# Kernel tuning notes

Measured on AMD Instinct MI355X. Metric: run time of the kernel, lower is better.

Reference implementation:

```python
import jax, jax.numpy as jnp
import numpy as np

N, D, H, L = 100000, 128, 4, 2
C = D // H  # per-head channels
E = 1600000
NEG_SLOPE = 0.2
LN_EPS = 1e-5


def setup_inputs() -> dict:
    key = jax.random.key(0)
    ks = jax.random.split(key, 8)
    x = jax.random.normal(ks[0], (N, D), dtype=jnp.float32)
    edge_index = jax.random.randint(ks[1], (2, E), 0, N, dtype=jnp.int64)
    s = 1.0 / np.sqrt(D)
    Wl = jax.random.normal(ks[2], (L, D, D), dtype=jnp.float32) * s
    Wr = jax.random.normal(ks[3], (L, D, D), dtype=jnp.float32) * s
    att = jax.random.normal(ks[4], (L, H, C), dtype=jnp.float32) * (1.0 / np.sqrt(C))
    bias = jnp.zeros((L, D), dtype=jnp.float32)
    gamma = jnp.ones((L, D), dtype=jnp.float32)
    beta = jnp.zeros((L, D), dtype=jnp.float32)
    return {"x": x, "edge_index": edge_index, "Wl": Wl, "Wr": Wr,
            "att": att, "bias": bias, "gamma": gamma, "beta": beta}


def _gatv2_layer(h, src, dst, Wl, Wr, att, bias):
    # h: (N, D); src/dst: (E2,) with self-loops already appended
    xl = (h @ Wl).reshape(N, H, C)  # source-side transform
    xr = (h @ Wr).reshape(N, H, C)  # target-side transform
    e = jax.nn.leaky_relu(xl[src] + xr[dst], NEG_SLOPE)      # (E2, H, C)
    alpha = jnp.einsum('ehc,hc->eh', e, att)                 # (E2, H)
    # segment softmax over incoming edges of each destination node
    m = jax.ops.segment_max(alpha, dst, num_segments=N)      # (N, H)
    ea = jnp.exp(alpha - m[dst])
    s = jax.ops.segment_sum(ea, dst, num_segments=N)         # (N, H)
    a = ea / s[dst]                                          # (E2, H)
    out = jax.ops.segment_sum(a[:, :, None] * xl[src], dst, num_segments=N)
    return out.reshape(N, D) + bias


def _layer_norm(y, gamma, beta):
    mu = jnp.mean(y, axis=-1, keepdims=True)
    var = jnp.var(y, axis=-1, keepdims=True)
    return (y - mu) * jax.lax.rsqrt(var + LN_EPS) * gamma + beta


def reference(x, edge_index, Wl, Wr, att, bias, gamma, beta):
    # PyG GATv2Conv defaults: add_self_loops=True (eval mode: dropouts identity)
    loops = jnp.arange(N, dtype=edge_index.dtype)
    src = jnp.concatenate([edge_index[0], loops])
    dst = jnp.concatenate([edge_index[1], loops])
    h = x
    for l in range(L):
        g = _gatv2_layer(h, src, dst, Wl[l], Wr[l], att[l], bias[l])
        h = h + jax.nn.elu(_layer_norm(g, gamma[l], beta[l]))
    return h
```

## Files before the change

### kernel.cpp

```cpp
#include <hip/hip_runtime.h>
#include <hip/hip_fp16.h>
#include <math.h>

#define N_NODES 100000
#define D_FEAT  128
#define E_EDGES 1600000
#define E2      (E_EDGES + N_NODES)
#define NEG_SLOPE 0.2f
#define LN_EPS    1e-5f

#define NB   391
#define TS   8192
#define NTIL ((E2 + TS - 1) / TS)

typedef __attribute__((ext_vector_type(4))) float floatx4;
typedef _Float16 h2 __attribute__((ext_vector_type(2)));
typedef _Float16 h8 __attribute__((ext_vector_type(8)));

static __device__ __forceinline__ float fdot2f(h2 a, h2 b, float c) {
#if __has_builtin(__builtin_amdgcn_fdot2)
    return __builtin_amdgcn_fdot2(a, b, c, false);
#else
    return (float)a[0] * (float)b[0] + (float)a[1] * (float)b[1] + c;
#endif
}

static __device__ __forceinline__ h2 shfl_xor_h2(h2 v, int off) {
    int i = __builtin_bit_cast(int, v);
    i = __shfl_xor(i, off);
    return __builtin_bit_cast(h2, i);
}

__global__ __launch_bounds__(1024) void tile_count(const int* __restrict__ edge_dst,
                                                   int* __restrict__ tcnt,
                                                   unsigned short* __restrict__ rankbuf) {
    __shared__ int h[NB];
    const int t = threadIdx.x;
    if (t < NB) h[t] = 0;
    __syncthreads();
    const int base = blockIdx.x * TS;
#pragma unroll
    for (int j = 0; j < TS / 1024; ++j) {
        int i = base + j * 1024 + t;
        if (i < E2) {
            int d = (i < E_EDGES) ? edge_dst[i] : (i - E_EDGES);
            int rk = atomicAdd(&h[d >> 8], 1);
            rankbuf[i] = (unsigned short)rk;
        }
    }
    __syncthreads();
    if (t < NB) tcnt[blockIdx.x * NB + t] = h[t];
}

__global__ __launch_bounds__(256) void col_scan(const int* __restrict__ tcnt,
                                                int* __restrict__ toff,
                                                int* __restrict__ bcnt) {
    __shared__ int s[256];
    const int b = blockIdx.x;
    const int t = threadIdx.x;
    int v = (t < NTIL) ? tcnt[t * NB + b] : 0;
    s[t] = v;
    __syncthreads();
    for (int off = 1; off < 256; off <<= 1) {
        int x = (t >= off) ? s[t - off] : 0;
        __syncthreads();
        s[t] += x;
        __syncthreads();
    }
    if (t < NTIL) toff[t * NB + b] = s[t] - v;
    if (t == 255) bcnt[b] = s[255];
}

__global__ __launch_bounds__(512) void bucket_scan(const int* __restrict__ bcnt,
                                                   int* __restrict__ bstart,
                                                   int* __restrict__ rowstart) {
    __shared__ int s[512];
    const int t = threadIdx.x;
    int v = (t < NB) ? bcnt[t] : 0;
    s[t] = v;
    __syncthreads();
    for (int off = 1; off < 512; off <<= 1) {
        int x = (t >= off) ? s[t - off] : 0;
        __syncthreads();
        s[t] += x;
        __syncthreads();
    }
    if (t <= NB) bstart[t] = s[t] - v;
    if (t == 0) rowstart[N_NODES] = E2;
}

__global__ __launch_bounds__(1024) void tile_scatter(const int* __restrict__ edge_src,
                                                     const int* __restrict__ edge_dst,
                                                     const int* __restrict__ bstart,
                                                     const int* __restrict__ toff,
                                                     const unsigned short* __restrict__ rankbuf,
                                                     unsigned* __restrict__ pairbuf) {
    __shared__ int base[NB];
    const int t = threadIdx.x;
    if (t < NB) base[t] = bstart[t] + toff[blockIdx.x * NB + t];
    __syncthreads();
    const int tb = blockIdx.x * TS;
#pragma unroll
    for (int j = 0; j < TS / 1024; ++j) {
        int i = tb + j * 1024 + t;
        if (i < E2) {
            int d, sr;
            if (i < E_EDGES) { d = edge_dst[i]; sr = edge_src[i]; }
            else             { d = i - E_EDGES; sr = d; }
            int b = d >> 8;
            int pos = base[b] + (int)rankbuf[i];
            pairbuf[pos] = (unsigned)sr | ((unsigned)(d & 255) << 17);
        }
    }
}

__global__ __launch_bounds__(1024) void bucketize(const unsigned* __restrict__ pairbuf,
                                                  const int* __restrict__ bstart,
                                                  int* __restrict__ rowstart,
                                                  int* __restrict__ csr_src) {
    __shared__ int cnt[256], off[256];
    const int blk = blockIdx.x;
    const int t = threadIdx.x;
    const int nbase = blk << 8;
    if (t < 256) cnt[t] = 0;
    __syncthreads();
    const int e0 = bstart[blk], e1 = bstart[blk + 1];

    unsigned pr0, pr1, pr2, pr3, pr4, pr5, pr6, pr7;
    int rk0, rk1, rk2, rk3, rk4, rk5, rk6, rk7;
#define LOADP(K, PR)  { int p = e0 + t + (K) * 1024; PR = (p < e1) ? pairbuf[p] : 0u; }
    LOADP(0, pr0) LOADP(1, pr1) LOADP(2, pr2) LOADP(3, pr3)
    LOADP(4, pr4) LOADP(5, pr5) LOADP(6, pr6) LOADP(7, pr7)
#undef LOADP
#define HIST(K, PR, RK) { int p = e0 + t + (K) * 1024; \
        RK = (p < e1) ? atomicAdd(&cnt[PR >> 17], 1) : 0; }
    HIST(0, pr0, rk0) HIST(1, pr1, rk1) HIST(2, pr2, rk2) HIST(3, pr3, rk3)
    HIST(4, pr4, rk4) HIST(5, pr5, rk5) HIST(6, pr6, rk6) HIST(7, pr7, rk7)
#undef HIST
    __syncthreads();

    int v = (t < 256) ? cnt[t] : 0;
    __shared__ int sc[256];
    if (t < 256) sc[t] = v;
    __syncthreads();
    for (int o = 1; o < 256; o <<= 1) {
        int x = (t < 256 && t >= o) ? sc[t - o] : 0;
        __syncthreads();
        if (t < 256) sc[t] += x;
        __syncthreads();
    }
    if (t < 256) {
        int excl = sc[t] - v;
        int node = nbase + t;
        if (node < N_NODES) rowstart[node] = e0 + excl;
        off[t] = e0 + excl;
    }
    __syncthreads();

#define SCAT(K, PR, RK) { int p = e0 + t + (K) * 1024; \
        if (p < e1) csr_src[off[PR >> 17] + RK] = (int)(PR & 0x1FFFF); }
    SCAT(0, pr0, rk0) SCAT(1, pr1, rk1) SCAT(2, pr2, rk2) SCAT(3, pr3, rk3)
    SCAT(4, pr4, rk4) SCAT(5, pr5, rk5) SCAT(6, pr6, rk6) SCAT(7, pr7, rk7)
#undef SCAT
}

__global__ void prep_wt(const float* __restrict__ Wl, const float* __restrict__ Wr,
                        const float* __restrict__ att,
                        _Float16* __restrict__ Wt, _Float16* __restrict__ atth) {
    int idx = blockIdx.x * 256 + threadIdx.x;
    if (idx < 65536) {
        int l    = idx >> 15;
        int rem  = idx & 32767;
        int side = rem >> 14;
        int cw   = rem & 16383;
        int col  = cw >> 7, k = cw & 127;
        const float* W = side ? Wr : Wl;
        Wt[idx] = (_Float16)W[l * 16384 + k * 128 + col];
    } else if (idx < 65536 + 256) {
        int j = idx - 65536;
        atth[j] = (_Float16)att[j];
    }
}

__global__ __launch_bounds__(256) void gemm_mfma5(
        const _Float16* __restrict__ hA,
        const float* __restrict__ Afp,
        const _Float16* __restrict__ Wt,
        _Float16* __restrict__ xl, _Float16* __restrict__ xr, int n_rows) {
    __shared__ char bsm[65536];
    const int tid  = threadIdx.x;
    const int wave = tid >> 6;
    const int lane = tid & 63;
    const int m = lane & 15;
    const int q = lane >> 4;
    const int r0 = (blockIdx.x * 4 + wave) * 32;

#pragma unroll
    for (int k = 0; k < 16; ++k) {
        int ci  = tid + k * 256;
        int row = ci >> 4;
        int off = (ci & 15) << 4;
        uint4 v = *(const uint4*)((const char*)Wt + row * 256 + off);
        *(uint4*)(bsm + row * 256 + (off ^ ((row & 7) << 4))) = v;
    }
    __syncthreads();

    int arow0 = r0 + m;        if (arow0 >= n_rows) arow0 = n_rows - 1;
    int arow1 = r0 + 16 + m;   if (arow1 >= n_rows) arow1 = n_rows - 1;

    floatx4 acc[2][2][8];
#pragma unroll
    for (int s = 0; s < 2; ++s)
#pragma unroll
        for (int rt = 0; rt < 2; ++rt)
#pragma unroll
            for (int ct = 0; ct < 8; ++ct) acc[s][rt][ct] = (floatx4){0.f,0.f,0.f,0.f};

    const int swz = (m & 7) << 4;
#pragma unroll
    for (int ks = 0; ks < 4; ++ks) {
        const int k0 = ks * 32 + q * 8;
        const int cb = k0 * 2;
        h8 a0, a1;
        if (Afp) {
            float4 f0 = *(const float4*)(Afp + (size_t)arow0 * 128 + k0);
            float4 f1 = *(const float4*)(Afp + (size_t)arow0 * 128 + k0 + 4);
            float4 g0 = *(const float4*)(Afp + (size_t)arow1 * 128 + k0);
            float4 g1 = *(const float4*)(Afp + (size_t)arow1 * 128 + k0 + 4);
            a0 = (h8){(_Float16)f0.x, (_Float16)f0.y, (_Float16)f0.z, (_Float16)f0.w,
                      (_Float16)f1.x, (_Float16)f1.y, (_Float16)f1.z, (_Float16)f1.w};
            a1 = (h8){(_Float16)g0.x, (_Float16)g0.y, (_Float16)g0.z, (_Float16)g0.w,
                      (_Float16)g1.x, (_Float16)g1.y, (_Float16)g1.z, (_Float16)g1.w};
        } else {
            a0 = *(const h8*)(hA + (size_t)arow0 * 128 + k0);
            a1 = *(const h8*)(hA + (size_t)arow1 * 128 + k0);
        }
#pragma unroll
        for (int s = 0; s < 2; ++s) {
#pragma unroll
            for (int ct = 0; ct < 8; ++ct) {
                int row = s * 128 + ct * 16 + m;
                h8 b = *(const h8*)(bsm + row * 256 + (cb ^ swz));
                acc[s][0][ct] = __builtin_amdgcn_mfma_f32_16x16x32_f16(a0, b, acc[s][0][ct], 0, 0, 0);
                acc[s][1][ct] = __builtin_amdgcn_mfma_f32_16x16x32_f16(a1, b, acc[s][1][ct], 0, 0, 0);
            }
        }
    }

#pragma unroll
    for (int s = 0; s < 2; ++s) {
        _Float16* out = s ? xr : xl;
#pragma unroll
        for (int rt = 0; rt < 2; ++rt)
#pragma unroll
            for (int ct = 0; ct < 8; ++ct)
#pragma unroll
                for (int i = 0; i < 4; ++i) {
                    int row = r0 + rt * 16 + q * 4 + i;
                    if (row < n_rows)
                        out[(size_t)row * 128 + ct * 16 + m] = (_Float16)acc[s][rt][ct][i];
                }
    }
}

union U16 { uint4 u; h2 h[4]; };

__global__ __launch_bounds__(256) void gat_node10(
        const _Float16* __restrict__ xl,
        const _Float16* __restrict__ xr,
        const float* __restrict__ h_in_f32,
        const _Float16* __restrict__ h_in_f16,
        const int* __restrict__ rowstart, const int* __restrict__ csr_src,
        const _Float16* __restrict__ atth, const float* __restrict__ bias,
        const float* __restrict__ gamma, const float* __restrict__ beta,
        float* __restrict__ out_f32,
        _Float16* __restrict__ out_f16) {
    const int wave = threadIdx.x >> 6;
    const int lane = threadIdx.x & 63;
    const int node = blockIdx.x * 4 + wave;
    const int esub = lane >> 3;
    const int r    = lane & 7;
    const int c0   = r * 16;
    const int c    = c0 + 2 * esub;

    const int p0 = rowstart[node], p1 = rowstart[node + 1];
    const int pe = p1 - 1;

    U16 xra, xrb, ata, atb;
    {
        const uint4* xp = (const uint4*)(xr + (size_t)node * 128 + c0);
        xra.u = xp[0]; xrb.u = xp[1];
        const uint4* ap = (const uint4*)(atth + c0);
        ata.u = ap[0]; atb.u = ap[1];
    }
    const float2 bi = *(const float2*)(bias + c);
    const h2 ns2 = {(_Float16)NEG_SLOPE, (_Float16)NEG_SLOPE};

    const unsigned short* xls = (const unsigned short*)xl;

    float s = 0.f;
    h2 acc2[8];
#pragma unroll
    for (int j = 0; j < 8; ++j) acc2[j] = (h2){(_Float16)0.f, (_Float16)0.f};

    auto consume = [&](const U16& u0, const U16& u1, bool v) {
        float da = 0.f, db = 0.f;
#pragma unroll
        for (int qq = 0; qq < 4; ++qq) {
            h2 z  = u0.h[qq] + xra.h[qq];
            h2 lk = __builtin_elementwise_max(z, z * ns2);
            da = fdot2f(lk, ata.h[qq], da);
        }
#pragma unroll
        for (int qq = 0; qq < 4; ++qq) {
            h2 z  = u1.h[qq] + xrb.h[qq];
            h2 lk = __builtin_elementwise_max(z, z * ns2);
            db = fdot2f(lk, atb.h[qq], db);
        }
        float d = da + db;
        float alpha = d + __shfl_xor(d, 1);
        float w = v ? __expf(alpha) : 0.f;
        s += w;
        h2 w2 = {(_Float16)w, (_Float16)w};
#pragma unroll
        for (int qq = 0; qq < 4; ++qq)
            acc2[qq] = w2 * u0.h[qq] + acc2[qq];
#pragma unroll
        for (int qq = 0; qq < 4; ++qq)
            acc2[qq + 4] = w2 * u1.h[qq] + acc2[qq + 4];
    };

    int pA = p0 + esub;        if (pA > pe) pA = pe;
    int pB = p0 + 8 + esub;    if (pB > pe) pB = pe;
    int pC = p0 + 16 + esub;   if (pC > pe) pC = pe;
    int i0 = csr_src[pA];
    int i1 = csr_src[pB];
    int i2 = csr_src[pC];

    U16 s0a, s0b, s1a, s1b, s2a, s2b;
    { const uint4* rp = (const uint4*)(xls + (size_t)i0 * 128 + c0); s0a.u = rp[0]; s0b.u = rp[1]; }
    { const uint4* rp = (const uint4*)(xls + (size_t)i1 * 128 + c0); s1a.u = rp[0]; s1b.u = rp[1]; }

    int pb = p0;
    for (;;) {
        {
            int pn = pb + 24 + esub; if (pn > pe) pn = pe;
            int inew = csr_src[pn];
            if (pb + 16 < p1) {
                const uint4* rp = (const uint4*)(xls + (size_t)i2 * 128 + c0);
                s2a.u = rp[0]; s2b.u = rp[1];
            }
            consume(s0a, s0b, (pb + esub) < p1);
            i0 = inew;
            pb += 8; if (pb >= p1) break;
        }
        {
            int pn = pb + 24 + esub; if (pn > pe) pn = pe;
            int inew = csr_src[pn];
            if (pb + 16 < p1) {
                const uint4* rp = (const uint4*)(xls + (size_t)i0 * 128 + c0);
                s0a.u = rp[0]; s0b.u = rp[1];
            }
            consume(s1a, s1b, (pb + esub) < p1);
            i1 = inew;
            pb += 8; if (pb >= p1) break;
        }
        {
            int pn = pb + 24 + esub; if (pn > pe) pn = pe;
            int inew = csr_src[pn];
            if (pb + 16 < p1) {
                const uint4* rp = (const uint4*)(xls + (size_t)i1 * 128 + c0);
                s1a.u = rp[0]; s1b.u = rp[1];
            }
            consume(s2a, s2b, (pb + esub) < p1);
            i2 = inew;
            pb += 8; if (pb >= p1) break;
        }
    }

    float ssum = s;
    ssum += __shfl_xor(ssum, 8);
    ssum += __shfl_xor(ssum, 16);
    ssum += __shfl_xor(ssum, 32);

    const bool sel0 = (esub & 1) != 0;
    const bool sel1 = ((esub >> 1) & 1) != 0;
    const bool sel2 = ((esub >> 2) & 1) != 0;
    h2 b4[4];
#pragma unroll
    for (int k = 0; k < 4; ++k) {
        h2 keep = sel0 ? acc2[2 * k + 1] : acc2[2 * k];
        h2 send = sel0 ? acc2[2 * k]     : acc2[2 * k + 1];
        b4[k] = keep + shfl_xor_h2(send, 8);
    }
    h2 c2[2];
#pragma unroll
    for (int k = 0; k < 2; ++k) {
        h2 keep = sel1 ? b4[2 * k + 1] : b4[2 * k];
        h2 send = sel1 ? b4[2 * k]     : b4[2 * k + 1];
        c2[k] = keep + shfl_xor_h2(send, 16);
    }
    h2 keepf = sel2 ? c2[1] : c2[0];
    h2 sendf = sel2 ? c2[0] : c2[1];
    h2 tot = keepf + shfl_xor_h2(sendf, 32);

    const float invS = 1.f / ssum;
    float g0 = (float)tot[0] * invS + bi.x;
    float g1 = (float)tot[1] * invS + bi.y;

    const float2 ga = *(const float2*)(gamma + c);
    const float2 be = *(const float2*)(beta + c);
    float hx, hy;
    if (h_in_f16) {
        h2 hv = *(const h2*)(h_in_f16 + (size_t)node * 128 + c);
        hx = (float)hv[0]; hy = (float)hv[1];
    } else {
        float2 hv = *(const float2*)(h_in_f32 + (size_t)node * 128 + c);
        hx = hv.x; hy = hv.y;
    }

    float sum = g0 + g1, sq = g0 * g0 + g1 * g1;
#pragma unroll
    for (int off = 1; off < 64; off <<= 1) {
        sum += __shfl_xor(sum, off);
        sq  += __shfl_xor(sq, off);
    }
    float mu   = sum * (1.f / 128.f);
    float var  = sq * (1.f / 128.f) - mu * mu;
    float rstd = rsqrtf(var + LN_EPS);
    float y0 = (g0 - mu) * rstd * ga.x + be.x;
    float y1 = (g1 - mu) * rstd * ga.y + be.y;
    float e0 = (y0 > 0.f) ? y0 : (__expf(y0) - 1.f);
    float e1 = (y1 > 0.f) ? y1 : (__expf(y1) - 1.f);

    float ox = hx + e0;
    float oy = hy + e1;
    if (out_f32) {
        float2 o; o.x = ox; o.y = oy;
        *(float2*)(out_f32 + (size_t)node * 128 + c) = o;
    } else {
        h2 po = {(_Float16)ox, (_Float16)oy};
        *(h2*)(out_f16 + (size_t)node * 128 + c) = po;
    }
}

extern "C" void kernel_launch(void* const* d_in, const int* in_sizes, int n_in,
                              void* d_out, int out_size, void* d_ws, size_t ws_size,
                              hipStream_t stream) {
    const float* x     = (const float*)d_in[0];
    const int*   eidx  = (const int*)d_in[1];
    const float* Wl    = (const float*)d_in[2];
    const float* Wr    = (const float*)d_in[3];
    const float* att   = (const float*)d_in[4];
    const float* bias  = (const float*)d_in[5];
    const float* gamma = (const float*)d_in[6];
    const float* beta  = (const float*)d_in[7];
    float* out = (float*)d_out;

    char* ws = (char*)d_ws;
    _Float16* xl = (_Float16*)ws;              ws += (size_t)N_NODES * 128 * 2;
    _Float16* xr = (_Float16*)ws;              ws += (size_t)N_NODES * 128 * 2;
    _Float16* h16 = (_Float16*)ws;             ws += (size_t)N_NODES * 128 * 2;
    _Float16* Wt  = (_Float16*)ws;             ws += (size_t)65536 * 2;
    _Float16* atth = (_Float16*)ws;            ws += 256 * 2;
    unsigned* pairbuf = (unsigned*)ws;         ws += (size_t)E2 * 4;
    unsigned short* rankbuf = (unsigned short*)ws; ws += (size_t)E2 * 2;
    int* tcnt     = (int*)ws; ws += (size_t)NTIL * NB * 4;
    int* toff     = (int*)ws; ws += (size_t)NTIL * NB * 4;
    int* bcnt     = (int*)ws; ws += (NB + 1) * 4;
    int* bstart   = (int*)ws; ws += (NB + 1) * 4;
    int* rowstart = (int*)ws; ws += (size_t)(N_NODES + 4) * 4;
    int* csr_src  = (int*)ws; ws += (size_t)E2 * 4;

    const int* edge_src = eidx;
    const int* edge_dst = eidx + E_EDGES;

    prep_wt<<<257, 256, 0, stream>>>(Wl, Wr, att, Wt, atth);

    tile_count<<<NTIL, 1024, 0, stream>>>(edge_dst, tcnt, rankbuf);
    col_scan<<<NB, 256, 0, stream>>>(tcnt, toff, bcnt);
    bucket_scan<<<1, 512, 0, stream>>>(bcnt, bstart, rowstart);
    tile_scatter<<<NTIL, 1024, 0, stream>>>(edge_src, edge_dst, bstart, toff,
                                            rankbuf, pairbuf);
    bucketize<<<NB, 1024, 0, stream>>>(pairbuf, bstart, rowstart, csr_src);

    const int gemm_gx = (N_NODES + 127) / 128;
    for (int l = 0; l < 2; ++l) {
        gemm_mfma5<<<gemm_gx, 256, 0, stream>>>(
            (l == 0) ? nullptr : h16, (l == 0) ? x : nullptr,
            Wt + (size_t)l * 32768, xl, xr, N_NODES);
        gat_node10<<<N_NODES / 4, 256, 0, stream>>>(
            xl, xr,
            (l == 0) ? x : nullptr, (l == 0) ? nullptr : h16,
            rowstart, csr_src,
            atth + l * 128, bias + l * 128, gamma + l * 128, beta + l * 128,
            (l == 1) ? out : nullptr, (l == 0) ? h16 : nullptr);
    }
}
```

Measured before the change: 364.7 us.

## Fuse CSR build and weight prep into one cooperative kernel with grid syncs

Replaces six small kernels (weight conversion, tile count, column scan, bucket scan, tile scatter, bucketize) with a single cooperative launch of 256 blocks of 1024 threads that uses grid.sync between phases. This removes five kernel launches and their inter-kernel gaps from the preprocessing stage. In exchange, the bucket loops now run over 256 persistent blocks instead of 391, the column scan uses a 1024-wide scan in place of a 256-wide one, and the kernel depends on all 256 blocks being co-resident.

```diff
diff --git a/kernel.cpp b/kernel.cpp
--- a/kernel.cpp
+++ b/kernel.cpp
@@ -1,6 +1,9 @@
 #include <hip/hip_runtime.h>
 #include <hip/hip_fp16.h>
+#include <hip/hip_cooperative_groups.h>
 #include <math.h>
+
+namespace cg = cooperative_groups;
 
 #define N_NODES 100000
 #define D_FEAT  128
@@ -31,154 +34,142 @@
     return __builtin_bit_cast(h2, i);
 }
 
-__global__ __launch_bounds__(1024) void tile_count(const int* __restrict__ edge_dst,
-                                                   int* __restrict__ tcnt,
-                                                   unsigned short* __restrict__ rankbuf) {
-    __shared__ int h[NB];
+__global__ __launch_bounds__(1024) void csr_fused(
+        const int* __restrict__ edge_src, const int* __restrict__ edge_dst,
+        const float* __restrict__ Wl, const float* __restrict__ Wr,
+        const float* __restrict__ att,
+        _Float16* __restrict__ Wt, _Float16* __restrict__ atth,
+        int* __restrict__ tcnt, int* __restrict__ toff,
+        int* __restrict__ bcnt, int* __restrict__ bstart,
+        unsigned short* __restrict__ rankbuf, unsigned* __restrict__ pairbuf,
+        int* __restrict__ rowstart, int* __restrict__ csr_src) {
+    cg::grid_group grid = cg::this_grid();
+    __shared__ int sh[1024];
+    __shared__ int sh2[256];
     const int t = threadIdx.x;
-    if (t < NB) h[t] = 0;
-    __syncthreads();
-    const int base = blockIdx.x * TS;
-#pragma unroll
-    for (int j = 0; j < TS / 1024; ++j) {
-        int i = base + j * 1024 + t;
-        if (i < E2) {
-            int d = (i < E_EDGES) ? edge_dst[i] : (i - E_EDGES);
-            int rk = atomicAdd(&h[d >> 8], 1);
-            rankbuf[i] = (unsigned short)rk;
-        }
-    }
-    __syncthreads();
-    if (t < NB) tcnt[blockIdx.x * NB + t] = h[t];
-}
-
-__global__ __launch_bounds__(256) void col_scan(const int* __restrict__ tcnt,
-                                                int* __restrict__ toff,
-                                                int* __restrict__ bcnt) {
-    __shared__ int s[256];
     const int b = blockIdx.x;
-    const int t = threadIdx.x;
-    int v = (t < NTIL) ? tcnt[t * NB + b] : 0;
-    s[t] = v;
-    __syncthreads();
-    for (int off = 1; off < 256; off <<= 1) {
-        int x = (t >= off) ? s[t - off] : 0;
-        __syncthreads();
-        s[t] += x;
-        __syncthreads();
-    }
-    if (t < NTIL) toff[t * NB + b] = s[t] - v;
-    if (t == 255) bcnt[b] = s[255];
-}
-
-__global__ __launch_bounds__(512) void bucket_scan(const int* __restrict__ bcnt,
-                                                   int* __restrict__ bstart,
-                                                   int* __restrict__ rowstart) {
-    __shared__ int s[512];
-    const int t = threadIdx.x;
-    int v = (t < NB) ? bcnt[t] : 0;
-    s[t] = v;
-    __syncthreads();
-    for (int off = 1; off < 512; off <<= 1) {
-        int x = (t >= off) ? s[t - off] : 0;
-        __syncthreads();
-        s[t] += x;
-        __syncthreads();
-    }
-    if (t <= NB) bstart[t] = s[t] - v;
-    if (t == 0) rowstart[N_NODES] = E2;
-}
-
-__global__ __launch_bounds__(1024) void tile_scatter(const int* __restrict__ edge_src,
-                                                     const int* __restrict__ edge_dst,
-                                                     const int* __restrict__ bstart,
-                                                     const int* __restrict__ toff,
-                                                     const unsigned short* __restrict__ rankbuf,
-                                                     unsigned* __restrict__ pairbuf) {
-    __shared__ int base[NB];
-    const int t = threadIdx.x;
-    if (t < NB) base[t] = bstart[t] + toff[blockIdx.x * NB + t];
-    __syncthreads();
-    const int tb = blockIdx.x * TS;
-#pragma unroll
-    for (int j = 0; j < TS / 1024; ++j) {
-        int i = tb + j * 1024 + t;
-        if (i < E2) {
-            int d, sr;
-            if (i < E_EDGES) { d = edge_dst[i]; sr = edge_src[i]; }
-            else             { d = i - E_EDGES; sr = d; }
-            int b = d >> 8;
-            int pos = base[b] + (int)rankbuf[i];
-            pairbuf[pos] = (unsigned)sr | ((unsigned)(d & 255) << 17);
-        }
-    }
-}
-
-__global__ __launch_bounds__(1024) void bucketize(const unsigned* __restrict__ pairbuf,
-                                                  const int* __restrict__ bstart,
-                                                  int* __restrict__ rowstart,
-                                                  int* __restrict__ csr_src) {
-    __shared__ int cnt[256], off[256];
-    const int blk = blockIdx.x;
-    const int t = threadIdx.x;
-    const int nbase = blk << 8;
-    if (t < 256) cnt[t] = 0;
-    __syncthreads();
-    const int e0 = bstart[blk], e1 = bstart[blk + 1];
-
-    unsigned pr0, pr1, pr2, pr3, pr4, pr5, pr6, pr7;
-    int rk0, rk1, rk2, rk3, rk4, rk5, rk6, rk7;
+
+    {
+        int gid = b * 1024 + t;
+        if (gid < 65536) {
+            int l = gid >> 15, rem = gid & 32767, side = rem >> 14, cw = rem & 16383;
+            int col = cw >> 7, k = cw & 127;
+            const float* W = side ? Wr : Wl;
+            Wt[gid] = (_Float16)W[l * 16384 + k * 128 + col];
+        } else if (gid < 65536 + 256) {
+            atth[gid - 65536] = (_Float16)att[gid - 65536];
+        }
+    }
+
+    if (b < NTIL) {
+        if (t < NB) sh[t] = 0;
+        __syncthreads();
+        const int base = b * TS;
+#pragma unroll
+        for (int j = 0; j < TS / 1024; ++j) {
+            int i = base + j * 1024 + t;
+            if (i < E2) {
+                int d = (i < E_EDGES) ? edge_dst[i] : (i - E_EDGES);
+                int rk = atomicAdd(&sh[d >> 8], 1);
+                rankbuf[i] = (unsigned short)rk;
+            }
+        }
+        __syncthreads();
+        if (t < NB) tcnt[b * NB + t] = sh[t];
+    }
+    grid.sync();
+
+    for (int bk = b; bk < NB; bk += 256) {
+        int v = (t < NTIL) ? tcnt[t * NB + bk] : 0;
+        sh[t] = v;
+        __syncthreads();
+        for (int off = 1; off < 1024; off <<= 1) {
+            int x = (t >= off) ? sh[t - off] : 0;
+            __syncthreads();
+            sh[t] += x;
+            __syncthreads();
+        }
+        if (t < NTIL) toff[t * NB + bk] = sh[t] - v;
+        if (t == 1023) bcnt[bk] = sh[1023];
+        __syncthreads();
+    }
+    grid.sync();
+
+    if (b == 0) {
+        int v = (t < NB) ? bcnt[t] : 0;
+        sh[t] = v;
+        __syncthreads();
+        for (int off = 1; off < 1024; off <<= 1) {
+            int x = (t >= off) ? sh[t - off] : 0;
+            __syncthreads();
+            sh[t] += x;
+            __syncthreads();
+        }
+        if (t <= NB) bstart[t] = sh[t] - v;
+        if (t == 0) rowstart[N_NODES] = E2;
+    }
+    grid.sync();
+
+    if (b < NTIL) {
+        if (t < NB) sh[t] = bstart[t] + toff[b * NB + t];
+        __syncthreads();
+        const int tb = b * TS;
+#pragma unroll
+        for (int j = 0; j < TS / 1024; ++j) {
+            int i = tb + j * 1024 + t;
+            if (i < E2) {
+                int d, sr;
+                if (i < E_EDGES) { d = edge_dst[i]; sr = edge_src[i]; }
+                else             { d = i - E_EDGES; sr = d; }
+                int bk = d >> 8;
+                pairbuf[sh[bk] + (int)rankbuf[i]] =
+                    (unsigned)sr | ((unsigned)(d & 255) << 17);
+            }
+        }
+    }
+    grid.sync();
+
+    for (int bk = b; bk < NB; bk += 256) {
+        if (t < 256) sh[t] = 0;
+        __syncthreads();
+        const int e0 = bstart[bk], e1 = bstart[bk + 1];
+
+        unsigned pr0, pr1, pr2, pr3, pr4, pr5, pr6, pr7;
+        int rk0, rk1, rk2, rk3, rk4, rk5, rk6, rk7;
 #define LOADP(K, PR)  { int p = e0 + t + (K) * 1024; PR = (p < e1) ? pairbuf[p] : 0u; }
-    LOADP(0, pr0) LOADP(1, pr1) LOADP(2, pr2) LOADP(3, pr3)
-    LOADP(4, pr4) LOADP(5, pr5) LOADP(6, pr6) LOADP(7, pr7)
+        LOADP(0, pr0) LOADP(1, pr1) LOADP(2, pr2) LOADP(3, pr3)
+        LOADP(4, pr4) LOADP(5, pr5) LOADP(6, pr6) LOADP(7, pr7)
 #undef LOADP
 #define HIST(K, PR, RK) { int p = e0 + t + (K) * 1024; \
-        RK = (p < e1) ? atomicAdd(&cnt[PR >> 17], 1) : 0; }
-    HIST(0, pr0, rk0) HIST(1, pr1, rk1) HIST(2, pr2, rk2) HIST(3, pr3, rk3)
-    HIST(4, pr4, rk4) HIST(5, pr5, rk5) HIST(6, pr6, rk6) HIST(7, pr7, rk7)
+        RK = (p < e1) ? atomicAdd(&sh[PR >> 17], 1) : 0; }
+        HIST(0, pr0, rk0) HIST(1, pr1, rk1) HIST(2, pr2, rk2) HIST(3, pr3, rk3)
+        HIST(4, pr4, rk4) HIST(5, pr5, rk5) HIST(6, pr6, rk6) HIST(7, pr7, rk7)
 #undef HIST
-    __syncthreads();
-
-    int v = (t < 256) ? cnt[t] : 0;
-    __shared__ int sc[256];
-    if (t < 256) sc[t] = v;
-    __syncthreads();
-    for (int o = 1; o < 256; o <<= 1) {
-        int x = (t < 256 && t >= o) ? sc[t - o] : 0;
-        __syncthreads();
-        if (t < 256) sc[t] += x;
-        __syncthreads();
-    }
-    if (t < 256) {
-        int excl = sc[t] - v;
-        int node = nbase + t;
-        if (node < N_NODES) rowstart[node] = e0 + excl;
-        off[t] = e0 + excl;
-    }
-    __syncthreads();
+        __syncthreads();
+
+        int v = (t < 256) ? sh[t] : 0;
+        if (t < 256) sh[256 + t] = v;
+        __syncthreads();
+        for (int o = 1; o < 256; o <<= 1) {
+            int x = (t < 256 && t >= o) ? sh[256 + t - o] : 0;
+            __syncthreads();
+            if (t < 256) sh[256 + t] += x;
+            __syncthreads();
+        }
+        if (t < 256) {
+            int excl = sh[256 + t] - v;
+            int node = (bk << 8) + t;
+            if (node < N_NODES) rowstart[node] = e0 + excl;
+            sh2[t] = e0 + excl;
+        }
+        __syncthreads();
 
 #define SCAT(K, PR, RK) { int p = e0 + t + (K) * 1024; \
-        if (p < e1) csr_src[off[PR >> 17] + RK] = (int)(PR & 0x1FFFF); }
-    SCAT(0, pr0, rk0) SCAT(1, pr1, rk1) SCAT(2, pr2, rk2) SCAT(3, pr3, rk3)
-    SCAT(4, pr4, rk4) SCAT(5, pr5, rk5) SCAT(6, pr6, rk6) SCAT(7, pr7, rk7)
+        if (p < e1) csr_src[sh2[PR >> 17] + RK] = (int)(PR & 0x1FFFF); }
+        SCAT(0, pr0, rk0) SCAT(1, pr1, rk1) SCAT(2, pr2, rk2) SCAT(3, pr3, rk3)
+        SCAT(4, pr4, rk4) SCAT(5, pr5, rk5) SCAT(6, pr6, rk6) SCAT(7, pr7, rk7)
 #undef SCAT
-}
-
-__global__ void prep_wt(const float* __restrict__ Wl, const float* __restrict__ Wr,
-                        const float* __restrict__ att,
-                        _Float16* __restrict__ Wt, _Float16* __restrict__ atth) {
-    int idx = blockIdx.x * 256 + threadIdx.x;
-    if (idx < 65536) {
-        int l    = idx >> 15;
-        int rem  = idx & 32767;
-        int side = rem >> 14;
-        int cw   = rem & 16383;
-        int col  = cw >> 7, k = cw & 127;
-        const float* W = side ? Wr : Wl;
-        Wt[idx] = (_Float16)W[l * 16384 + k * 128 + col];
-    } else if (idx < 65536 + 256) {
-        int j = idx - 65536;
-        atth[j] = (_Float16)att[j];
+        __syncthreads();
     }
 }
 
@@ -240,9 +231,9 @@
 #pragma unroll
             for (int ct = 0; ct < 8; ++ct) {
                 int row = s * 128 + ct * 16 + m;
-                h8 b = *(const h8*)(bsm + row * 256 + (cb ^ swz));
-                acc[s][0][ct] = __builtin_amdgcn_mfma_f32_16x16x32_f16(a0, b, acc[s][0][ct], 0, 0, 0);
-                acc[s][1][ct] = __builtin_amdgcn_mfma_f32_16x16x32_f16(a1, b, acc[s][1][ct], 0, 0, 0);
+                h8 bfrag = *(const h8*)(bsm + row * 256 + (cb ^ swz));
+                acc[s][0][ct] = __builtin_amdgcn_mfma_f32_16x16x32_f16(a0, bfrag, acc[s][0][ct], 0, 0, 0);
+                acc[s][1][ct] = __builtin_amdgcn_mfma_f32_16x16x32_f16(a1, bfrag, acc[s][1][ct], 0, 0, 0);
             }
         }
     }
@@ -475,14 +466,14 @@
     const int* edge_src = eidx;
     const int* edge_dst = eidx + E_EDGES;
 
-    prep_wt<<<257, 256, 0, stream>>>(Wl, Wr, att, Wt, atth);
-
-    tile_count<<<NTIL, 1024, 0, stream>>>(edge_dst, tcnt, rankbuf);
-    col_scan<<<NB, 256, 0, stream>>>(tcnt, toff, bcnt);
-    bucket_scan<<<1, 512, 0, stream>>>(bcnt, bstart, rowstart);
-    tile_scatter<<<NTIL, 1024, 0, stream>>>(edge_src, edge_dst, bstart, toff,
-                                            rankbuf, pairbuf);
-    bucketize<<<NB, 1024, 0, stream>>>(pairbuf, bstart, rowstart, csr_src);
+    void* cargs[] = {
+        (void*)&edge_src, (void*)&edge_dst, (void*)&Wl, (void*)&Wr, (void*)&att,
+        (void*)&Wt, (void*)&atth, (void*)&tcnt, (void*)&toff, (void*)&bcnt,
+        (void*)&bstart, (void*)&rankbuf, (void*)&pairbuf, (void*)&rowstart,
+        (void*)&csr_src
+    };
+    hipLaunchCooperativeKernel((void*)csr_fused, dim3(256), dim3(1024),
+                               cargs, 0, stream);
 
     const int gemm_gx = (N_NODES + 127) / 128;
     for (int l = 0; l < 2; ++l) {
```

Measured after the change: 503.0 us. 1.38x slower.
